# Performance work log

Hardware: AMD Instinct MI355X
Metric: run time of the kernel (lower is better)

The kernel has to match this reference:

```python
import jax, jax.numpy as jnp
import numpy as np

EPS = 0.1
TANH_SCALE = 1.0
B, T, N, D, C, DE = 8, 120, 24, 48, 1128, 256  # C = D*(D-1)//2


def setup_inputs() -> dict:
    key = jax.random.key(0)
    k1, k2, k3, k4 = jax.random.split(key, 4)
    x = jax.random.normal(k1, (B, T, N, D), dtype=jnp.float32)
    context = jax.random.normal(k2, (B, C, N, DE), dtype=jnp.float32)
    Wkv = jax.random.normal(k3, (D, DE), dtype=jnp.float32) * (DE ** -0.5)
    bkv = jax.random.normal(k4, (D,), dtype=jnp.float32) * 0.01
    return {"x": x, "context": context, "Wkv": Wkv, "bkv": bkv}


def reference(x, context, Wkv, bkv):
    # x: [B,T,N,D], context: [B,C,N,DE]
    b, t, n, d = x.shape
    kv = jnp.einsum('bcne,de->bcnd', context, Wkv) + bkv      # [B,C,N,D]
    kv = jnp.transpose(kv, (0, 2, 3, 1))                      # [B,N,D,C]
    xt = jnp.transpose(x, (0, 2, 1, 3))                       # [B,N,T,D]
    sp = jnp.einsum('bntd,bndc->bntc', xt, kv)                # [B,N,T,C]
    sp = EPS * TANH_SCALE * jnp.tanh(sp / TANH_SCALE)
    i, j = jnp.tril_indices(d, k=-1)
    A = jnp.zeros((b, n, t, d, d), dtype=x.dtype).at[..., i, j].set(sp)
    A = A - jnp.swapaxes(A, -1, -2)                           # skew-symmetric
    dx = jnp.einsum('bntd,bntde->bnte', xt, A)                # per-(B,N,T) matvec
    y = xt + dx
    return jnp.transpose(y, (0, 2, 1, 3))                     # [B,T,N,D]
```

## Files before the change

kernel.cpp:

```cpp
#include <hip/hip_runtime.h>
#include <hip/hip_bf16.h>


constexpr int Bc = 8, Tc = 120, Nc = 24, Dc = 48, Cc = 1128, DEc = 256;
constexpr int BNc = Bc * Nc;
constexpr int KVP = 48;

using short8 = __attribute__((ext_vector_type(8))) short;
using f32x4  = __attribute__((ext_vector_type(4))) float;

__device__ __forceinline__ ushort f2b(float f) {
    union { float f; unsigned u; } v; v.f = f;
    unsigned r = (v.u + 0x7fffu + ((v.u >> 16) & 1u)) >> 16;
    return (ushort)r;
}
__device__ __forceinline__ float b2f(ushort u) {
    union { unsigned q; float f; } cv; cv.q = ((unsigned)u) << 16; return cv.f;
}
__device__ __forceinline__ short bcast(float f) {
    return (short)__bfloat16_as_ushort(__float2bfloat16(f));
}
__device__ __forceinline__ short8 pack8(const float4& a, const float4& b) {
    short8 r;
    r[0] = bcast(a.x); r[1] = bcast(a.y); r[2] = bcast(a.z); r[3] = bcast(a.w);
    r[4] = bcast(b.x); r[5] = bcast(b.y); r[6] = bcast(b.z); r[7] = bcast(b.w);
    return r;
}

constexpr int SWs = 264;
__global__ __launch_bounds__(256) void k1_kv(const float* __restrict__ ctx,
                                             const float* __restrict__ Wkv,
                                             const float* __restrict__ bkv,
                                             ushort* __restrict__ kvb) {
    __shared__ ushort sW[Dc * SWs];
    const int bn = blockIdx.x, c0 = blockIdx.y * 128;
    const int b = bn / Nc, n = bn % Nc;
    const int tid = threadIdx.x, wave = tid >> 6, lane = tid & 63;
    const int tr = lane & 15, kg = lane >> 4;
    const float* ctxb = ctx + ((size_t)b * Cc * Nc + n) * DEc;

    for (int l = tid; l < Dc * 64; l += 256) {
        int d = l >> 6, e = (l & 63) << 2;
        float4 w = *reinterpret_cast<const float4*>(Wkv + d * DEc + e);
        ushort4 u;
        u.x = (ushort)bcast(w.x); u.y = (ushort)bcast(w.y);
        u.z = (ushort)bcast(w.z); u.w = (ushort)bcast(w.w);
        *reinterpret_cast<ushort4*>(&sW[d * SWs + e]) = u;
    }

    const float* crow[2];
    #pragma unroll
    for (int cn = 0; cn < 2; ++cn) {
        int c = c0 + wave * 32 + cn * 16 + tr;
        crow[cn] = ctxb + (size_t)(c < Cc ? c : Cc - 1) * (Nc * DEc);
    }

    f32x4 acc[3][2];
    #pragma unroll
    for (int mf = 0; mf < 3; ++mf)
        #pragma unroll
        for (int cn = 0; cn < 2; ++cn) acc[mf][cn] = (f32x4){0.f, 0.f, 0.f, 0.f};

    __syncthreads();

    #pragma unroll
    for (int ks = 0; ks < 8; ++ks) {
        const int e0 = ks * 32 + kg * 8;
        short8 bfrag[2];
        #pragma unroll
        for (int cn = 0; cn < 2; ++cn) {
            float4 a0 = *reinterpret_cast<const float4*>(crow[cn] + e0);
            float4 a1 = *reinterpret_cast<const float4*>(crow[cn] + e0 + 4);
            bfrag[cn] = pack8(a0, a1);
        }
        short8 afrag[3];
        #pragma unroll
        for (int mf = 0; mf < 3; ++mf)
            afrag[mf] = *reinterpret_cast<const short8*>(&sW[(mf * 16 + tr) * SWs + e0]);
        #pragma unroll
        for (int mf = 0; mf < 3; ++mf)
            #pragma unroll
            for (int cn = 0; cn < 2; ++cn)
                acc[mf][cn] = __builtin_amdgcn_mfma_f32_16x16x32_bf16(afrag[mf], bfrag[cn], acc[mf][cn], 0, 0, 0);
    }

    float4 bias[3];
    #pragma unroll
    for (int mf = 0; mf < 3; ++mf)
        bias[mf] = *reinterpret_cast<const float4*>(bkv + mf * 16 + kg * 4);
    #pragma unroll
    for (int cn = 0; cn < 2; ++cn) {
        int c = c0 + wave * 32 + cn * 16 + tr;
        if (c < Cc) {
            ushort* dst = kvb + ((size_t)bn * Cc + c) * KVP;
            #pragma unroll
            for (int mf = 0; mf < 3; ++mf) {
                ushort4 u;
                u.x = f2b(acc[mf][cn][0] + bias[mf].x);
                u.y = f2b(acc[mf][cn][1] + bias[mf].y);
                u.z = f2b(acc[mf][cn][2] + bias[mf].z);
                u.w = f2b(acc[mf][cn][3] + bias[mf].w);
                *reinterpret_cast<ushort4*>(dst + mf * 16 + kg * 4) = u;
            }
        }
    }
}

constexpr int TT4 = 30;
constexpr int SG2 = 1140;
__global__ __launch_bounds__(256, 2) void k2_fused(const float* __restrict__ x,
                                                   const ushort* __restrict__ kvb,
                                                   float* __restrict__ out) {
    __shared__ ushort sG[TT4 * SG2];
    __shared__ float  sXf[TT4 * 52];
    __shared__ ushort sXb[32 * 72];
    const int L = blockIdx.x;
    const int bn = (L & 7) + 8 * (L >> 5);
    const int tt = (L >> 3) & 3;
    const int b = bn / Nc, n = bn % Nc, t0 = tt * TT4;
    const int tid = threadIdx.x, wave = tid >> 6, lane = tid & 63;
    const int tr = lane & 15, kg = lane >> 4;

    if (tid < 180) {
        int t = tid / 6, q = tid % 6;
        *reinterpret_cast<ushort4*>(&sXb[t * 72 + 48 + q * 4]) = make_ushort4(0, 0, 0, 0);
    } else if (tid < 198) {
        int l = tid - 180;
        *reinterpret_cast<short8*>(&sXb[30 * 72 + l * 8]) = (short8){0, 0, 0, 0, 0, 0, 0, 0};
    }
    for (int l = tid; l < TT4 * 12; l += 256)
        sG[(l / 12) * SG2 + 1128 + (l % 12)] = 0;
    for (int l = tid; l < TT4 * 12; l += 256) {
        int t = l / 12, dv = (l % 12) * 4;
        float4 v = *reinterpret_cast<const float4*>(x + (((size_t)b * Tc + t0 + t) * Nc + n) * Dc + dv);
        *reinterpret_cast<float4*>(&sXf[t * 52 + dv]) = v;
        *reinterpret_cast<ushort4*>(&sXb[t * 72 + dv]) = make_ushort4(f2b(v.x), f2b(v.y), f2b(v.z), f2b(v.w));
    }
    __syncthreads();
    const short8 af0 = *reinterpret_cast<const short8*>(&sXb[tr * 72 + kg * 8]);
    const short8 af1 = *reinterpret_cast<const short8*>(&sXb[tr * 72 + 32 + kg * 8]);
    const short8 ag0 = *reinterpret_cast<const short8*>(&sXb[(16 + tr) * 72 + kg * 8]);
    const short8 ag1 = *reinterpret_cast<const short8*>(&sXb[(16 + tr) * 72 + 32 + kg * 8]);

    const ushort* kvbn = kvb + (size_t)bn * Cc * KVP;
    short8 b0, b1, p0, p1;
    {
        int c = wave * 16 + tr;
        const ushort* p = kvbn + (size_t)c * KVP + kg * 8;
        b0 = *reinterpret_cast<const short8*>(p);
        b1 = *reinterpret_cast<const short8*>(p + 32);
    }
    #pragma unroll
    for (int u = 0; u < 18; ++u) {
        if (u < 17) {
            int c = (wave + (u + 1) * 4) * 16 + tr; if (c > Cc - 1) c = Cc - 1;
            const ushort* p = kvbn + (size_t)c * KVP + kg * 8;
            p0 = *reinterpret_cast<const short8*>(p);
            p1 = *reinterpret_cast<const short8*>(p + 32);
        }
        f32x4 alo = (f32x4){0.f, 0.f, 0.f, 0.f};
        f32x4 ahi = (f32x4){0.f, 0.f, 0.f, 0.f};
        alo = __builtin_amdgcn_mfma_f32_16x16x32_bf16(af0, b0, alo, 0, 0, 0);
        alo = __builtin_amdgcn_mfma_f32_16x16x32_bf16(af1, b1, alo, 0, 0, 0);
        ahi = __builtin_amdgcn_mfma_f32_16x16x32_bf16(ag0, b0, ahi, 0, 0, 0);
        ahi = __builtin_amdgcn_mfma_f32_16x16x32_bf16(ag1, b1, ahi, 0, 0, 0);
        int c = (wave + u * 4) * 16 + tr;
        if (c < Cc) {
            #pragma unroll
            for (int r = 0; r < 4; ++r) {
                int tl = kg * 4 + r;
                float glo = 0.1f - 0.2f * __builtin_amdgcn_rcpf(__expf(2.0f * alo[r]) + 1.0f);
                sG[tl * SG2 + c] = f2b(glo);
                if (tl + 16 < TT4) {
                    float ghi = 0.1f - 0.2f * __builtin_amdgcn_rcpf(__expf(2.0f * ahi[r]) + 1.0f);
                    sG[(tl + 16) * SG2 + c] = f2b(ghi);
                }
            }
        }
        b0 = p0; b1 = p1;
    }
    __syncthreads();

    int ea[6], ta[6], tea[6];
    float dxa[6];
    #pragma unroll
    for (int p = 0; p < 6; ++p) {
        int idx = tid + p * 256;
        if (idx >= TT4 * 48) idx = TT4 * 48 - 1;
        ta[p] = idx / 48; ea[p] = idx % 48;
        tea[p] = ea[p] * (ea[p] - 1) / 2;
        dxa[p] = 0.f;
    }
    int td = 0;
    #pragma unroll 4
    for (int d = 0; d < 48; ++d) {
        #pragma unroll
        for (int p = 0; p < 6; ++p) {
            bool gt = d > ea[p];
            int c = gt ? (td + ea[p]) : (tea[p] + d);
            float gv = b2f(sG[ta[p] * SG2 + c]);
            float xv = sXf[ta[p] * 52 + d];
            float m = gt ? xv : -xv;
            if (d == ea[p]) m = 0.f;
            dxa[p] = fmaf(m, gv, dxa[p]);
        }
        td += d;
    }
    #pragma unroll
    for (int p = 0; p < 6; ++p) {
        int idx = tid + p * 256;
        if (idx < TT4 * 48)
            out[(((size_t)b * Tc + t0 + ta[p]) * Nc + n) * Dc + ea[p]] = sXf[ta[p] * 52 + ea[p]] + dxa[p];
    }
}

extern "C" void kernel_launch(void* const* d_in, const int* in_sizes, int n_in,
                              void* d_out, int out_size, void* d_ws, size_t ws_size,
                              hipStream_t stream) {
    (void)in_sizes; (void)n_in; (void)out_size; (void)ws_size;
    const float* x   = (const float*)d_in[0];
    const float* ctx = (const float*)d_in[1];
    const float* Wkv = (const float*)d_in[2];
    const float* bkv = (const float*)d_in[3];
    float* out   = (float*)d_out;
    ushort* kvb  = (ushort*)d_ws;

    k1_kv<<<dim3(BNc, 9), dim3(256), 0, stream>>>(ctx, Wkv, bkv, kvb);
    k2_fused<<<dim3(BNc * 4), dim3(256), 0, stream>>>(x, kvb, out);
}
```

Baseline: 85.92 us.

## Reassociate the projection so x·Wkv is precomputed and context is consumed directly

The order of the two contractions is swapped. A new first kernel computes x·Wkv (T×DE per (b,n)) in bf16, plus the x·bias term. The fused kernel then multiplies those rows directly against the fp32 context, converted to bf16 on the fly. This removes the kv intermediate write and read, and the separate context pass. The cost is that context is now read by each of the four time-tile blocks per (b,n), and the MFMA work on the DE dimension rises from 48 to 120 rows per context row.

Result: slower. 131.3 us (+52.8%).

```diff
diff --git a/kernel.cpp b/kernel.cpp
--- a/kernel.cpp
+++ b/kernel.cpp
@@ -4,7 +4,6 @@
 
 constexpr int Bc = 8, Tc = 120, Nc = 24, Dc = 48, Cc = 1128, DEc = 256;
 constexpr int BNc = Bc * Nc;
-constexpr int KVP = 48;
 
 using short8 = __attribute__((ext_vector_type(8))) short;
 using f32x4  = __attribute__((ext_vector_type(4))) float;
@@ -27,81 +26,60 @@
     return r;
 }
 
-constexpr int SWs = 264;
-__global__ __launch_bounds__(256) void k1_kv(const float* __restrict__ ctx,
+constexpr int WTs = 64;
+constexpr int XBs = 72;
+__global__ __launch_bounds__(256) void k0_xw(const float* __restrict__ x,
                                              const float* __restrict__ Wkv,
                                              const float* __restrict__ bkv,
-                                             ushort* __restrict__ kvb) {
-    __shared__ ushort sW[Dc * SWs];
-    const int bn = blockIdx.x, c0 = blockIdx.y * 128;
-    const int b = bn / Nc, n = bn % Nc;
+                                             ushort* __restrict__ xw,
+                                             float* __restrict__ spb) {
+    __shared__ ushort sWT[256 * WTs];
+    __shared__ ushort sXb[128 * XBs];
+    const int bn = blockIdx.x, b = bn / Nc, n = bn % Nc;
     const int tid = threadIdx.x, wave = tid >> 6, lane = tid & 63;
     const int tr = lane & 15, kg = lane >> 4;
-    const float* ctxb = ctx + ((size_t)b * Cc * Nc + n) * DEc;
-
-    for (int l = tid; l < Dc * 64; l += 256) {
-        int d = l >> 6, e = (l & 63) << 2;
-        float4 w = *reinterpret_cast<const float4*>(Wkv + d * DEc + e);
-        ushort4 u;
-        u.x = (ushort)bcast(w.x); u.y = (ushort)bcast(w.y);
-        u.z = (ushort)bcast(w.z); u.w = (ushort)bcast(w.w);
-        *reinterpret_cast<ushort4*>(&sW[d * SWs + e]) = u;
-    }
-
-    const float* crow[2];
-    #pragma unroll
-    for (int cn = 0; cn < 2; ++cn) {
-        int c = c0 + wave * 32 + cn * 16 + tr;
-        crow[cn] = ctxb + (size_t)(c < Cc ? c : Cc - 1) * (Nc * DEc);
-    }
-
-    f32x4 acc[3][2];
-    #pragma unroll
-    for (int mf = 0; mf < 3; ++mf)
-        #pragma unroll
-        for (int cn = 0; cn < 2; ++cn) acc[mf][cn] = (f32x4){0.f, 0.f, 0.f, 0.f};
-
-    __syncthreads();
-
-    #pragma unroll
-    for (int ks = 0; ks < 8; ++ks) {
-        const int e0 = ks * 32 + kg * 8;
-        short8 bfrag[2];
-        #pragma unroll
-        for (int cn = 0; cn < 2; ++cn) {
-            float4 a0 = *reinterpret_cast<const float4*>(crow[cn] + e0);
-            float4 a1 = *reinterpret_cast<const float4*>(crow[cn] + e0 + 4);
-            bfrag[cn] = pack8(a0, a1);
-        }
-        short8 afrag[3];
-        #pragma unroll
-        for (int mf = 0; mf < 3; ++mf)
-            afrag[mf] = *reinterpret_cast<const short8*>(&sW[(mf * 16 + tr) * SWs + e0]);
-        #pragma unroll
-        for (int mf = 0; mf < 3; ++mf)
+    const float* xb = x + ((size_t)b * Tc * Nc + n) * Dc;
+
+    for (int l = tid; l < (256 * WTs) / 8; l += 256)
+        *reinterpret_cast<short8*>(&sWT[l * 8]) = (short8){0, 0, 0, 0, 0, 0, 0, 0};
+    for (int l = tid; l < (128 * XBs) / 8; l += 256)
+        *reinterpret_cast<short8*>(&sXb[l * 8]) = (short8){0, 0, 0, 0, 0, 0, 0, 0};
+    __syncthreads();
+    for (int l = tid; l < Dc * DEc; l += 256) {
+        int d = l >> 8, e = l & 255;
+        sWT[e * WTs + d] = f2b(Wkv[l]);
+    }
+    for (int l = tid; l < 128 * 12; l += 256) {
+        int t = l / 12, dv = (l % 12) * 4;
+        int tg = t < Tc ? t : Tc - 1;
+        float4 v = *reinterpret_cast<const float4*>(xb + (size_t)tg * Nc * Dc + dv);
+        *reinterpret_cast<ushort4*>(&sXb[t * XBs + dv]) =
+            make_ushort4(f2b(v.x), f2b(v.y), f2b(v.z), f2b(v.w));
+    }
+    __syncthreads();
+    if (tid < 128) {
+        int tg = tid < Tc ? tid : Tc - 1;
+        float a = 0.f;
+        #pragma unroll
+        for (int d = 0; d < Dc; ++d) a += xb[(size_t)tg * Nc * Dc + d] * bkv[d];
+        spb[(size_t)bn * 128 + tid] = a;
+    }
+    ushort* xwb = xw + (size_t)bn * (128 * 256);
+    #pragma unroll
+    for (int mi = 0; mi < 2; ++mi) {
+        const int m = wave + mi * 4;
+        short8 a0 = *reinterpret_cast<const short8*>(&sXb[(m * 16 + tr) * XBs + kg * 8]);
+        short8 a1 = *reinterpret_cast<const short8*>(&sXb[(m * 16 + tr) * XBs + 32 + kg * 8]);
+        #pragma unroll
+        for (int nf = 0; nf < 16; ++nf) {
+            short8 b0 = *reinterpret_cast<const short8*>(&sWT[(nf * 16 + tr) * WTs + kg * 8]);
+            short8 b1 = *reinterpret_cast<const short8*>(&sWT[(nf * 16 + tr) * WTs + 32 + kg * 8]);
+            f32x4 acc = (f32x4){0.f, 0.f, 0.f, 0.f};
+            acc = __builtin_amdgcn_mfma_f32_16x16x32_bf16(a0, b0, acc, 0, 0, 0);
+            acc = __builtin_amdgcn_mfma_f32_16x16x32_bf16(a1, b1, acc, 0, 0, 0);
             #pragma unroll
-            for (int cn = 0; cn < 2; ++cn)
-                acc[mf][cn] = __builtin_amdgcn_mfma_f32_16x16x32_bf16(afrag[mf], bfrag[cn], acc[mf][cn], 0, 0, 0);
-    }
-
-    float4 bias[3];
-    #pragma unroll
-    for (int mf = 0; mf < 3; ++mf)
-        bias[mf] = *reinterpret_cast<const float4*>(bkv + mf * 16 + kg * 4);
-    #pragma unroll
-    for (int cn = 0; cn < 2; ++cn) {
-        int c = c0 + wave * 32 + cn * 16 + tr;
-        if (c < Cc) {
-            ushort* dst = kvb + ((size_t)bn * Cc + c) * KVP;
-            #pragma unroll
-            for (int mf = 0; mf < 3; ++mf) {
-                ushort4 u;
-                u.x = f2b(acc[mf][cn][0] + bias[mf].x);
-                u.y = f2b(acc[mf][cn][1] + bias[mf].y);
-                u.z = f2b(acc[mf][cn][2] + bias[mf].z);
-                u.w = f2b(acc[mf][cn][3] + bias[mf].w);
-                *reinterpret_cast<ushort4*>(dst + mf * 16 + kg * 4) = u;
-            }
+            for (int r = 0; r < 4; ++r)
+                xwb[(m * 16 + kg * 4 + r) * 256 + nf * 16 + tr] = f2b(acc[r]);
         }
     }
 }
@@ -109,11 +87,12 @@
 constexpr int TT4 = 30;
 constexpr int SG2 = 1140;
 __global__ __launch_bounds__(256, 2) void k2_fused(const float* __restrict__ x,
-                                                   const ushort* __restrict__ kvb,
+                                                   const float* __restrict__ ctx,
+                                                   const ushort* __restrict__ xw,
+                                                   const float* __restrict__ spb,
                                                    float* __restrict__ out) {
     __shared__ ushort sG[TT4 * SG2];
     __shared__ float  sXf[TT4 * 52];
-    __shared__ ushort sXb[32 * 72];
     const int L = blockIdx.x;
     const int bn = (L & 7) + 8 * (L >> 5);
     const int tt = (L >> 3) & 3;
@@ -121,63 +100,53 @@
     const int tid = threadIdx.x, wave = tid >> 6, lane = tid & 63;
     const int tr = lane & 15, kg = lane >> 4;
 
-    if (tid < 180) {
-        int t = tid / 6, q = tid % 6;
-        *reinterpret_cast<ushort4*>(&sXb[t * 72 + 48 + q * 4]) = make_ushort4(0, 0, 0, 0);
-    } else if (tid < 198) {
-        int l = tid - 180;
-        *reinterpret_cast<short8*>(&sXb[30 * 72 + l * 8]) = (short8){0, 0, 0, 0, 0, 0, 0, 0};
-    }
     for (int l = tid; l < TT4 * 12; l += 256)
         sG[(l / 12) * SG2 + 1128 + (l % 12)] = 0;
     for (int l = tid; l < TT4 * 12; l += 256) {
         int t = l / 12, dv = (l % 12) * 4;
         float4 v = *reinterpret_cast<const float4*>(x + (((size_t)b * Tc + t0 + t) * Nc + n) * Dc + dv);
         *reinterpret_cast<float4*>(&sXf[t * 52 + dv]) = v;
-        *reinterpret_cast<ushort4*>(&sXb[t * 72 + dv]) = make_ushort4(f2b(v.x), f2b(v.y), f2b(v.z), f2b(v.w));
-    }
-    __syncthreads();
-    const short8 af0 = *reinterpret_cast<const short8*>(&sXb[tr * 72 + kg * 8]);
-    const short8 af1 = *reinterpret_cast<const short8*>(&sXb[tr * 72 + 32 + kg * 8]);
-    const short8 ag0 = *reinterpret_cast<const short8*>(&sXb[(16 + tr) * 72 + kg * 8]);
-    const short8 ag1 = *reinterpret_cast<const short8*>(&sXb[(16 + tr) * 72 + 32 + kg * 8]);
-
-    const ushort* kvbn = kvb + (size_t)bn * Cc * KVP;
-    short8 b0, b1, p0, p1;
-    {
-        int c = wave * 16 + tr;
-        const ushort* p = kvbn + (size_t)c * KVP + kg * 8;
-        b0 = *reinterpret_cast<const short8*>(p);
-        b1 = *reinterpret_cast<const short8*>(p + 32);
-    }
-    #pragma unroll
+    }
+    if (tid < TT4)
+        sXf[tid * 52 + 48] = spb[(size_t)bn * 128 + t0 + tid];
+    const ushort* xwb = xw + (size_t)bn * (128 * 256);
+    short8 af[8], ag[8];
+    #pragma unroll
+    for (int ks = 0; ks < 8; ++ks) {
+        af[ks] = *reinterpret_cast<const short8*>(&xwb[(size_t)(t0 + tr) * 256 + ks * 32 + kg * 8]);
+        ag[ks] = *reinterpret_cast<const short8*>(&xwb[(size_t)(t0 + 16 + tr) * 256 + ks * 32 + kg * 8]);
+    }
+    __syncthreads();
+
+    const float* ctxb = ctx + ((size_t)b * Cc * Nc + n) * DEc;
     for (int u = 0; u < 18; ++u) {
-        if (u < 17) {
-            int c = (wave + (u + 1) * 4) * 16 + tr; if (c > Cc - 1) c = Cc - 1;
-            const ushort* p = kvbn + (size_t)c * KVP + kg * 8;
-            p0 = *reinterpret_cast<const short8*>(p);
-            p1 = *reinterpret_cast<const short8*>(p + 32);
-        }
+        int c = (wave + u * 4) * 16 + tr;
+        int ce = c < Cc ? c : Cc - 1;
+        const float* crow = ctxb + (size_t)ce * (Nc * DEc);
         f32x4 alo = (f32x4){0.f, 0.f, 0.f, 0.f};
         f32x4 ahi = (f32x4){0.f, 0.f, 0.f, 0.f};
-        alo = __builtin_amdgcn_mfma_f32_16x16x32_bf16(af0, b0, alo, 0, 0, 0);
-        alo = __builtin_amdgcn_mfma_f32_16x16x32_bf16(af1, b1, alo, 0, 0, 0);
-        ahi = __builtin_amdgcn_mfma_f32_16x16x32_bf16(ag0, b0, ahi, 0, 0, 0);
-        ahi = __builtin_amdgcn_mfma_f32_16x16x32_bf16(ag1, b1, ahi, 0, 0, 0);
-        int c = (wave + u * 4) * 16 + tr;
+        #pragma unroll
+        for (int ks = 0; ks < 8; ++ks) {
+            float4 q0 = *reinterpret_cast<const float4*>(crow + ks * 32 + kg * 8);
+            float4 q1 = *reinterpret_cast<const float4*>(crow + ks * 32 + kg * 8 + 4);
+            short8 bf = pack8(q0, q1);
+            alo = __builtin_amdgcn_mfma_f32_16x16x32_bf16(af[ks], bf, alo, 0, 0, 0);
+            ahi = __builtin_amdgcn_mfma_f32_16x16x32_bf16(ag[ks], bf, ahi, 0, 0, 0);
+        }
         if (c < Cc) {
             #pragma unroll
             for (int r = 0; r < 4; ++r) {
                 int tl = kg * 4 + r;
-                float glo = 0.1f - 0.2f * __builtin_amdgcn_rcpf(__expf(2.0f * alo[r]) + 1.0f);
-                sG[tl * SG2 + c] = f2b(glo);
+                float slo = alo[r] + sXf[tl * 52 + 48];
+                float g = 0.1f - 0.2f * __builtin_amdgcn_rcpf(__expf(2.0f * slo) + 1.0f);
+                sG[tl * SG2 + c] = f2b(g);
                 if (tl + 16 < TT4) {
-                    float ghi = 0.1f - 0.2f * __builtin_amdgcn_rcpf(__expf(2.0f * ahi[r]) + 1.0f);
-                    sG[(tl + 16) * SG2 + c] = f2b(ghi);
+                    float shi = ahi[r] + sXf[(tl + 16) * 52 + 48];
+                    float gh = 0.1f - 0.2f * __builtin_amdgcn_rcpf(__expf(2.0f * shi) + 1.0f);
+                    sG[(tl + 16) * SG2 + c] = f2b(gh);
                 }
             }
         }
-        b0 = p0; b1 = p1;
     }
     __syncthreads();
 
@@ -222,9 +191,10 @@
     const float* ctx = (const float*)d_in[1];
     const float* Wkv = (const float*)d_in[2];
     const float* bkv = (const float*)d_in[3];
-    float* out   = (float*)d_out;
-    ushort* kvb  = (ushort*)d_ws;
-
-    k1_kv<<<dim3(BNc, 9), dim3(256), 0, stream>>>(ctx, Wkv, bkv, kvb);
-    k2_fused<<<dim3(BNc * 4), dim3(256), 0, stream>>>(x, kvb, out);
-}
+    float* out = (float*)d_out;
+    ushort* xw = (ushort*)d_ws;
+    float* spb = (float*)((char*)d_ws + 12582912);
+
+    k0_xw<<<dim3(BNc), dim3(256), 0, stream>>>(x, Wkv, bkv, xw, spb);
+    k2_fused<<<dim3(BNc * 4), dim3(256), 0, stream>>>(x, ctx, xw, spb, out);
+}
```
